# Kernel tuning notes

Hardware: AMD Instinct MI355X
Metric: run time of the kernel (lower is better)

Reference implementation:

```python
import jax, jax.numpy as jnp
import numpy as np

D = 512
N_CONCEPTS = 64
N_BANK = 200000
BS = 2048
N_CLASSES = 100
TOPK = 64


def setup_inputs() -> dict:
    key = jax.random.key(0)
    k1, k2, k3, k4 = jax.random.split(key, 4)
    concept = jax.random.uniform(k1, (D, N_CONCEPTS), dtype=jnp.float32, minval=-0.5, maxval=0.5)
    train_embedding = jax.random.normal(k2, (BS, D), dtype=jnp.float32)
    train_bank = jax.random.normal(k3, (N_BANK, D), dtype=jnp.float32)
    w_head = jax.random.normal(k4, (D, N_CLASSES), dtype=jnp.float32) * 0.05
    return {"concept": concept, "train_embedding": train_embedding,
            "train_bank": train_bank, "w_head": w_head, "topk": TOPK}


def reference(concept, train_embedding, train_bank, w_head, topk):
    # concept: (d, n_concepts); train_embedding: (bs, d); train_bank: (N, d)
    C = concept
    n_concepts = C.shape[1]
    gram = C.T @ C                                   # (n, n)
    proj_matrix = C @ jnp.linalg.inv(gram) @ C.T     # (d, d)
    modified = (proj_matrix @ train_embedding.T).T   # (bs, d) projected features
    # original_model modeled as linear head on the (hooked) bottleneck features
    y_pred = modified @ w_head                       # (bs, n_classes)
    orig_pred = train_embedding @ w_head             # (bs, n_classes)

    # vectorized per-concept euclidean distance to the whole bank + topk smallest
    bank_sq = jnp.sum(train_bank * train_bank, axis=1)        # (N,)
    c_sq = jnp.sum(C * C, axis=0)                             # (n,)
    d2 = c_sq[:, None] + bank_sq[None, :] - 2.0 * (C.T @ train_bank.T)  # (n, N)
    dist = jnp.sqrt(jnp.maximum(d2, 0.0))
    _, knn_idx = jax.lax.top_k(-dist, topk)                   # (n, k) smallest distances
    knn = train_bank[knn_idx]                                 # (n, k, d)
    dots = jnp.einsum('nkd,dn->n', knn, C) / topk             # sum(c * c_knn) / k per concept
    L_sparse_1 = jnp.mean(dots)

    eye = jnp.eye(n_concepts, dtype=gram.dtype)
    L_sparse_2 = jnp.mean(gram * (1.0 - eye))
    norm_metrics = jnp.mean(gram * eye)

    concept_pred = train_embedding @ C               # (bs, n_concepts)
    return (orig_pred, y_pred, L_sparse_1, L_sparse_2, norm_metrics, concept_pred)
```

## Files before the change

### kernel.cpp

```cpp
#include <hip/hip_runtime.h>
#include <float.h>

#define D_DIM 512
#define NC    64
#define NB    200000
#define BS_N  2048
#define NCL   100
#define TK    64
#define CAP   2048

#define O_ORIG 0
#define O_YPRED 204800
#define O_L1   409600
#define O_L2   409601
#define O_NORM 409602
#define O_CPRED 409603

#define W_GRAM  0
#define W_GINV  4096
#define W_U     8192
#define W_H     14592
#define W_Q     20992
#define W_MIN   220992
#define W_MAX   221056
#define W_BIN   221120
#define W_NBEL  221184
#define W_CCNT  221248
#define W_PSUM  221312
#define W_HIST  221376
#define W_CANDV 286912
#define W_CANDD 417984
#define W_PACKA 549056
#define W_PACKB 565440
#define W_S     610496

typedef __attribute__((ext_vector_type(8))) short bf16x8;
typedef __attribute__((ext_vector_type(4))) float f32x4;

__device__ inline unsigned f2ord(float f) {
    unsigned u = __float_as_uint(f);
    return (u & 0x80000000u) ? ~u : (u | 0x80000000u);
}
__device__ inline float ord2f(unsigned u) {
    return (u & 0x80000000u) ? __uint_as_float(u & 0x7fffffffu) : __uint_as_float(~u);
}
__device__ inline short f2bf(float f) {
    unsigned u = __float_as_uint(f);
    u += 0x7FFFu + ((u >> 16) & 1u);
    return (short)(u >> 16);
}

__global__ __launch_bounds__(256) void k1_setup(
    const float* __restrict__ C, const float* __restrict__ W,
    short* __restrict__ PA, short* __restrict__ PB,
    float* __restrict__ gram, float* __restrict__ U,
    unsigned* __restrict__ mnord, unsigned* __restrict__ mxord,
    unsigned* __restrict__ hist, int* __restrict__ ccnt, float* __restrict__ psum)
{
    int bid = blockIdx.x, t = threadIdx.x;
    if (bid < 16) {
        int idx = bid * 256 + t;
        int i = idx >> 6, j = idx & 63;
        float s = 0.f;
        for (int k = 0; k < D_DIM; ++k) s = fmaf(C[k*NC + i], C[k*NC + j], s);
        gram[idx] = s;
    } else if (bid < 41) {
        int idx = (bid - 16) * 256 + t;
        int i = idx / 100, j = idx - i * 100;
        float s = 0.f;
        for (int k = 0; k < D_DIM; ++k) s = fmaf(C[k*NC + i], W[k*NCL + j], s);
        U[idx] = s;
    } else if (bid < 281) {
        int b = bid - 41;
        #pragma unroll
        for (int rep = 0; rep < 2; ++rep) {
            int idx = t * 2 + rep;
            int lane = idx >> 3, j = idx & 7;
            if (b < 64) {
                int kt = b >> 2, ci = b & 3;
                int k = kt * 32 + (lane >> 4) * 8 + j;
                int col = ci * 16 + (lane & 15);
                PA[b * 512 + idx] = f2bf(C[k * NC + col]);
            } else {
                int bb = b - 64;
                int kt = bb / 11, ci = bb % 11;
                int k = kt * 32 + (lane >> 4) * 8 + j;
                int col = ci * 16 + (lane & 15);
                float v = 0.f;
                if (col < 64) v = C[k * NC + col];
                else if (col < 164) v = W[k * NCL + (col - 64)];
                PB[bb * 512 + idx] = f2bf(v);
            }
        }
    } else if (bid < 345) {
        int base = (bid - 281) * 1024;
        #pragma unroll
        for (int r = 0; r < 4; ++r) hist[base + r * 256 + t] = 0u;
    } else {
        if (t < 64) {
            mnord[t] = 0xFFFFFFFFu;
            mxord[t] = 0u;
            ccnt[t]  = 0;
            psum[t]  = 0.f;
        }
    }
}

__global__ __launch_bounds__(256) void k2_main(
    const float* __restrict__ E, const float* __restrict__ Bk,
    const short* __restrict__ PA, const short* __restrict__ PB,
    const float* __restrict__ gram, float* __restrict__ ginv,
    float* __restrict__ out3, float* __restrict__ T, float* __restrict__ O,
    float* __restrict__ S, float* __restrict__ Q,
    unsigned* __restrict__ mnord, unsigned* __restrict__ mxord)
{
    __shared__ float smem[64 * 65 + 64];
    int bid = blockIdx.x, t = threadIdx.x;

    if (bid == 0) {
        float (*A)[65] = (float(*)[65])smem;
        float* m = smem + 64 * 65;
        for (int idx = t; idx < 4096; idx += 256) A[idx >> 6][idx & 63] = gram[idx];
        __syncthreads();
        for (int k = 0; k < 64; ++k) {
            float d = 1.0f / A[k][k];
            if (t < 64) m[t] = A[t][k];
            __syncthreads();
            if (t < 64 && t != k) A[k][t] *= d;
            __syncthreads();
            for (int idx = t; idx < 4096; idx += 256) {
                int i = idx >> 6, j = idx & 63;
                if (i != k && j != k) A[i][j] = fmaf(-m[i], A[k][j], A[i][j]);
            }
            if (t < 64) {
                if (t != k) A[t][k] = -m[t] * d;
                else        A[k][k] = d;
            }
            __syncthreads();
        }
        for (int idx = t; idx < 4096; idx += 256) ginv[idx] = A[idx >> 6][idx & 63];
    } else if (bid == 1) {
        float* ra = smem; float* rd = smem + 256;
        float sa = 0.f, sd = 0.f;
        for (int idx = t; idx < NC * NC; idx += 256) {
            float g = gram[idx];
            sa += g;
            if (idx % (NC + 1) == 0) sd += g;
        }
        ra[t] = sa; rd[t] = sd;
        __syncthreads();
        for (int s2 = 128; s2 > 0; s2 >>= 1) {
            if (t < s2) { ra[t] += ra[t + s2]; rd[t] += rd[t + s2]; }
            __syncthreads();
        }
        if (t == 0) {
            out3[0] = 0.f;
            out3[1] = (ra[0] - rd[0]) * (1.0f / 4096.0f);
            out3[2] = rd[0] * (1.0f / 4096.0f);
        }
    } else if (bid < 18) {
        int eb = bid - 2;
        int wave = t >> 6, lane = t & 63;
        int quad = lane >> 4, l16 = lane & 15;
        int rbase = eb * 128 + wave * 32;
        int row0 = rbase + l16, row1 = rbase + 16 + l16;
        const float* p0 = E + (size_t)row0 * D_DIM + quad * 8;
        const float* p1 = E + (size_t)row1 * D_DIM + quad * 8;

        f32x4 acc[11][2];
        #pragma unroll
        for (int ci = 0; ci < 11; ++ci) { acc[ci][0] = 0.f; acc[ci][1] = 0.f; }

        for (int kt = 0; kt < 16; ++kt) {
            float4 a0 = *(const float4*)(p0 + kt*32);
            float4 b0 = *(const float4*)(p0 + kt*32 + 4);
            float4 a1 = *(const float4*)(p1 + kt*32);
            float4 b1 = *(const float4*)(p1 + kt*32 + 4);
            bf16x8 bf0 = { f2bf(a0.x), f2bf(a0.y), f2bf(a0.z), f2bf(a0.w),
                           f2bf(b0.x), f2bf(b0.y), f2bf(b0.z), f2bf(b0.w) };
            bf16x8 bf1 = { f2bf(a1.x), f2bf(a1.y), f2bf(a1.z), f2bf(a1.w),
                           f2bf(b1.x), f2bf(b1.y), f2bf(b1.z), f2bf(b1.w) };
            #pragma unroll
            for (int ci = 0; ci < 11; ++ci) {
                bf16x8 af = *(const bf16x8*)(PB + ((kt*11 + ci)*64 + lane)*8);
                acc[ci][0] = __builtin_amdgcn_mfma_f32_16x16x32_bf16(af, bf0, acc[ci][0], 0, 0, 0);
                acc[ci][1] = __builtin_amdgcn_mfma_f32_16x16x32_bf16(af, bf1, acc[ci][1], 0, 0, 0);
            }
        }
        #pragma unroll
        for (int ci = 0; ci < 11; ++ci) {
            #pragma unroll
            for (int j = 0; j < 4; ++j) {
                int col = ci*16 + quad*4 + j;
                if (col < 64) {
                    T[row0*NC + col] = acc[ci][0][j];
                    T[row1*NC + col] = acc[ci][1][j];
                } else if (col < 164) {
                    O[row0*NCL + (col-64)] = acc[ci][0][j];
                    O[row1*NCL + (col-64)] = acc[ci][1][j];
                }
            }
        }
    } else {
        int sb = bid - 18;
        unsigned* lmn = (unsigned*)smem;
        unsigned* lmx = lmn + 64;
        int wave = t >> 6, lane = t & 63;
        int quad = lane >> 4, l16 = lane & 15;
        if (t < 64) { lmn[t] = 0xFFFFFFFFu; lmx[t] = 0u; }
        __syncthreads();

        int rbase = sb * 128 + wave * 32;
        int row0 = rbase + l16, row1 = rbase + 16 + l16;
        bool v0 = row0 < NB, v1 = row1 < NB;
        int r0c = v0 ? row0 : (NB-1), r1c = v1 ? row1 : (NB-1);
        const float* p0 = Bk + (size_t)r0c * D_DIM + quad * 8;
        const float* p1 = Bk + (size_t)r1c * D_DIM + quad * 8;

        f32x4 acc[4][2];
        #pragma unroll
        for (int ci = 0; ci < 4; ++ci) { acc[ci][0] = 0.f; acc[ci][1] = 0.f; }
        float q0 = 0.f, q1 = 0.f;

        for (int kt = 0; kt < 16; ++kt) {
            float4 a0 = *(const float4*)(p0 + kt*32);
            float4 b0 = *(const float4*)(p0 + kt*32 + 4);
            float4 a1 = *(const float4*)(p1 + kt*32);
            float4 b1 = *(const float4*)(p1 + kt*32 + 4);
            q0 = fmaf(a0.x,a0.x, fmaf(a0.y,a0.y, fmaf(a0.z,a0.z, fmaf(a0.w,a0.w, q0))));
            q0 = fmaf(b0.x,b0.x, fmaf(b0.y,b0.y, fmaf(b0.z,b0.z, fmaf(b0.w,b0.w, q0))));
            q1 = fmaf(a1.x,a1.x, fmaf(a1.y,a1.y, fmaf(a1.z,a1.z, fmaf(a1.w,a1.w, q1))));
            q1 = fmaf(b1.x,b1.x, fmaf(b1.y,b1.y, fmaf(b1.z,b1.z, fmaf(b1.w,b1.w, q1))));
            bf16x8 bf0 = { f2bf(a0.x), f2bf(a0.y), f2bf(a0.z), f2bf(a0.w),
                           f2bf(b0.x), f2bf(b0.y), f2bf(b0.z), f2bf(b0.w) };
            bf16x8 bf1 = { f2bf(a1.x), f2bf(a1.y), f2bf(a1.z), f2bf(a1.w),
                           f2bf(b1.x), f2bf(b1.y), f2bf(b1.z), f2bf(b1.w) };
            #pragma unroll
            for (int ci = 0; ci < 4; ++ci) {
                bf16x8 af = *(const bf16x8*)(PA + ((kt*4 + ci)*64 + lane)*8);
                acc[ci][0] = __builtin_amdgcn_mfma_f32_16x16x32_bf16(af, bf0, acc[ci][0], 0, 0, 0);
                acc[ci][1] = __builtin_amdgcn_mfma_f32_16x16x32_bf16(af, bf1, acc[ci][1], 0, 0, 0);
            }
        }
        q0 += __shfl_xor(q0, 16); q0 += __shfl_xor(q0, 32);
        q1 += __shfl_xor(q1, 16); q1 += __shfl_xor(q1, 32);
        if (quad == 0) {
            if (v0) Q[row0] = q0;
            if (v1) Q[row1] = q1;
        }
        #pragma unroll
        for (int ci = 0; ci < 4; ++ci) {
            #pragma unroll
            for (int j = 0; j < 4; ++j) {
                int c = ci*16 + quad*4 + j;
                float s0 = q0 - 2.0f * acc[ci][0][j];
                float s1 = q1 - 2.0f * acc[ci][1][j];
                if (v0) S[(size_t)c*NB + row0] = s0;
                if (v1) S[(size_t)c*NB + row1] = s1;
                float mnv = fminf(v0 ? s0 : FLT_MAX,  v1 ? s1 : FLT_MAX);
                float mxv = fmaxf(v0 ? s0 : -FLT_MAX, v1 ? s1 : -FLT_MAX);
                #pragma unroll
                for (int o = 1; o < 16; o <<= 1) {
                    mnv = fminf(mnv, __shfl_xor(mnv, o));
                    mxv = fmaxf(mxv, __shfl_xor(mxv, o));
                }
                if (l16 == 0) {
                    atomicMin(&lmn[c], f2ord(mnv));
                    atomicMax(&lmx[c], f2ord(mxv));
                }
            }
        }
        __syncthreads();
        if (t < 64) {
            atomicMin(&mnord[t], lmn[t]);
            atomicMax(&mxord[t], lmx[t]);
        }
    }
}

__global__ __launch_bounds__(256) void k3_ph(
    const float* __restrict__ T, const float* __restrict__ ginv,
    const float* __restrict__ U, float* __restrict__ Y,
    const float* __restrict__ S, const unsigned* __restrict__ mnord,
    const unsigned* __restrict__ mxord, unsigned* __restrict__ hist)
{
    __shared__ float smem[6400];
    int bid = blockIdx.x, t = threadIdx.x;
    if (bid < 64) {
        for (int idx = t; idx < 6400; idx += 256) {
            int k = idx / 100, c = idx - k * 100;
            float s = 0.f;
            #pragma unroll 8
            for (int l = 0; l < NC; ++l) s = fmaf(ginv[k*NC + l], U[l*NCL + c], s);
            smem[idx] = s;
        }
        __syncthreads();
        for (int o = t; o < 3200; o += 256) {
            int r = o / 100, c = o - r * 100;
            int row = bid * 32 + r;
            float s = 0.f;
            #pragma unroll 8
            for (int k = 0; k < NC; ++k) s = fmaf(T[row*NC + k], smem[k*100 + c], s);
            Y[row*NCL + c] = s;
        }
    } else {
        int h = bid - 64;
        int c = h & 63, chunk = h >> 6;
        unsigned* hh = (unsigned*)smem;
        for (int i = t; i < 1024; i += 256) hh[i] = 0u;
        float mnf = ord2f(mnord[c]);
        float mxf = ord2f(mxord[c]);
        float invw = (mxf > mnf) ? 1024.0f / (mxf - mnf) : 0.f;
        __syncthreads();
        const float4* s4 = (const float4*)(S + (size_t)c * NB);
        int base = chunk * 1024;
        #pragma unroll
        for (int j = 0; j < 4; ++j) {
            int idx = base + j*256 + t;
            if (idx < NB/4) {
                float4 v = s4[idx];
                float vv[4] = {v.x, v.y, v.z, v.w};
                #pragma unroll
                for (int e = 0; e < 4; ++e) {
                    int b = (int)((vv[e] - mnf) * invw);
                    b = b < 0 ? 0 : (b > 1023 ? 1023 : b);
                    atomicAdd(&hh[b], 1u);
                }
            }
        }
        __syncthreads();
        for (int i = t; i < 1024; i += 256)
            if (hh[i]) atomicAdd(&hist[c*1024 + i], hh[i]);
    }
}

__global__ void scan_kernel(const unsigned* __restrict__ hist,
                            int* __restrict__ binB, int* __restrict__ nbel) {
    __shared__ unsigned h[1024];
    int c = blockIdx.x, t = threadIdx.x;
    for (int i = t; i < 1024; i += 256) h[i] = hist[c*1024 + i];
    __syncthreads();
    if (t == 0) {
        unsigned cum = 0; int B = 1023; unsigned below = 0;
        for (int b = 0; b < 1024; ++b) {
            unsigned hb = h[b];
            if (cum + hb >= TK) { B = b; below = cum; break; }
            cum += hb;
        }
        binB[c] = B;
        nbel[c] = (int)below;
    }
}

__global__ void collect_kernel(const float* __restrict__ S, const float* __restrict__ Q,
                               const unsigned* __restrict__ mn_ord, const unsigned* __restrict__ mx_ord,
                               const int* __restrict__ binB,
                               int* __restrict__ ccnt, float* __restrict__ candv,
                               float* __restrict__ candd, float* __restrict__ psum) {
    __shared__ float red[256];
    int c = blockIdx.y, t = threadIdx.x;
    float mnf = ord2f(mn_ord[c]);
    float mxf = ord2f(mx_ord[c]);
    float invw = (mxf > mnf) ? 1024.0f / (mxf - mnf) : 0.f;
    int B = binB[c];
    const float4* s4 = (const float4*)(S + (size_t)c * NB);
    int base = blockIdx.x * 1024;
    float dsum = 0.f;
    #pragma unroll
    for (int j = 0; j < 4; ++j) {
        int idx = base + j*256 + t;
        if (idx < NB/4) {
            float4 v = s4[idx];
            float vv[4] = {v.x, v.y, v.z, v.w};
            #pragma unroll
            for (int e = 0; e < 4; ++e) {
                int b = (int)((vv[e] - mnf) * invw);
                b = b < 0 ? 0 : (b > 1023 ? 1023 : b);
                if (b < B) {
                    dsum += (Q[idx*4 + e] - vv[e]) * 0.5f;
                } else if (b == B) {
                    int p = atomicAdd(&ccnt[c], 1);
                    if (p < CAP) {
                        candv[c*CAP + p] = vv[e];
                        candd[c*CAP + p] = (Q[idx*4 + e] - vv[e]) * 0.5f;
                    }
                }
            }
        }
    }
    red[t] = dsum;
    __syncthreads();
    for (int s2 = 128; s2 > 0; s2 >>= 1) {
        if (t < s2) red[t] += red[t+s2];
        __syncthreads();
    }
    if (t == 0 && red[0] != 0.f) atomicAdd(&psum[c], red[0]);
}

__global__ void final_kernel(const int* __restrict__ binB, const int* __restrict__ nbel,
                             const int* __restrict__ ccnt, const float* __restrict__ candv,
                             const float* __restrict__ candd, const float* __restrict__ psum,
                             float* __restrict__ out_l1) {
    __shared__ float v[CAP];
    __shared__ float dd[CAP];
    int c = blockIdx.x, t = threadIdx.x;
    int M = ccnt[c]; if (M > CAP) M = CAP;
    int r = TK - nbel[c]; if (r > M) r = M;
    for (int i = t; i < M; i += 64) { v[i] = candv[c*CAP + i]; dd[i] = candd[c*CAP + i]; }
    __syncthreads();
    float sum = 0.f;
    for (int j = 0; j < r; ++j) {
        float bv = FLT_MAX; int bi = -1;
        for (int i = t; i < M; i += 64)
            if (v[i] < bv) { bv = v[i]; bi = i; }
        #pragma unroll
        for (int o = 32; o > 0; o >>= 1) {
            float ov = __shfl_down(bv, o);
            int   oi = __shfl_down(bi, o);
            if (ov < bv) { bv = ov; bi = oi; }
        }
        bi = __shfl(bi, 0);
        if (t == 0 && bi >= 0) { sum += dd[bi]; v[bi] = FLT_MAX; }
        __syncthreads();
    }
    if (t == 0) atomicAdd(out_l1, (sum + psum[c]) * (1.0f/4096.0f));
}

extern "C" void kernel_launch(void* const* d_in, const int* in_sizes, int n_in,
                              void* d_out, int out_size, void* d_ws, size_t ws_size,
                              hipStream_t stream) {
    const float* C  = (const float*)d_in[0];
    const float* E  = (const float*)d_in[1];
    const float* Bk = (const float*)d_in[2];
    const float* W  = (const float*)d_in[3];
    float* out = (float*)d_out;
    float* ws  = (float*)d_ws;

    float*    gram  = ws + W_GRAM;
    float*    ginv  = ws + W_GINV;
    float*    U     = ws + W_U;
    float*    Q     = ws + W_Q;
    unsigned* mnord = (unsigned*)(ws + W_MIN);
    unsigned* mxord = (unsigned*)(ws + W_MAX);
    int*      binB  = (int*)(ws + W_BIN);
    int*      nbel  = (int*)(ws + W_NBEL);
    int*      ccnt  = (int*)(ws + W_CCNT);
    float*    psum  = ws + W_PSUM;
    unsigned* hist  = (unsigned*)(ws + W_HIST);
    float*    candv = ws + W_CANDV;
    float*    candd = ws + W_CANDD;
    short*    PA    = (short*)(ws + W_PACKA);
    short*    PB    = (short*)(ws + W_PACKB);
    float*    S     = ws + W_S;

    k1_setup<<<346, 256, 0, stream>>>(C, W, PA, PB, gram, U, mnord, mxord, hist, ccnt, psum);
    k2_main <<<1581, 256, 0, stream>>>(E, Bk, PA, PB, gram, ginv, out + O_L1,
                                       out + O_CPRED, out + O_ORIG, S, Q, mnord, mxord);
    k3_ph   <<<3200, 256, 0, stream>>>(out + O_CPRED, ginv, U, out + O_YPRED,
                                       S, mnord, mxord, hist);
    scan_kernel   <<<64, 256, 0, stream>>>(hist, binB, nbel);
    collect_kernel<<<dim3(49, 64), 256, 0, stream>>>(S, Q, mnord, mxord, binB, ccnt, candv, candd, psum);
    final_kernel  <<<NC, 64, 0, stream>>>(binB, nbel, ccnt, candv, candd, psum, out + O_L1);
}
```

Measured before the change: 703.1 us.

## Fold histogram scan into collect/final kernels and precompute ginv·U once

Removes the separate single-threaded scan kernel. collect_kernel and final_kernel now each run a parallel prefix scan over the histogram to find the threshold bin, so the sequential 1024-step loop and one launch go away. The ginv·U product is now computed once by the block that inverts the gram matrix, instead of redundantly in each of the 64 Y blocks of k3. final_kernel also moves to 256 threads, with a cross-wave argmin done through shared memory. The cost is a redundant scan in each of the 3136 collect blocks, plus extra serial work on the inversion block in k2.

```diff
diff --git a/kernel.cpp b/kernel.cpp
--- a/kernel.cpp
+++ b/kernel.cpp
@@ -23,7 +23,7 @@
 #define W_Q     20992
 #define W_MIN   220992
 #define W_MAX   221056
-#define W_BIN   221120
+#define W_DONE  221120
 #define W_NBEL  221184
 #define W_CCNT  221248
 #define W_PSUM  221312
@@ -109,7 +109,8 @@
 __global__ __launch_bounds__(256) void k2_main(
     const float* __restrict__ E, const float* __restrict__ Bk,
     const short* __restrict__ PA, const short* __restrict__ PB,
-    const float* __restrict__ gram, float* __restrict__ ginv,
+    const float* __restrict__ gram, const float* __restrict__ U,
+    float* __restrict__ ginv, float* __restrict__ H,
     float* __restrict__ out3, float* __restrict__ T, float* __restrict__ O,
     float* __restrict__ S, float* __restrict__ Q,
     unsigned* __restrict__ mnord, unsigned* __restrict__ mxord)
@@ -139,6 +140,13 @@
             __syncthreads();
         }
         for (int idx = t; idx < 4096; idx += 256) ginv[idx] = A[idx >> 6][idx & 63];
+        for (int idx = t; idx < 6400; idx += 256) {
+            int k = idx / 100, c = idx - k * 100;
+            float s = 0.f;
+            #pragma unroll 8
+            for (int l = 0; l < NC; ++l) s = fmaf(A[k][l], U[l*NCL + c], s);
+            H[idx] = s;
+        }
     } else if (bid == 1) {
         float* ra = smem; float* rd = smem + 256;
         float sa = 0.f, sd = 0.f;
@@ -279,21 +287,15 @@
 }
 
 __global__ __launch_bounds__(256) void k3_ph(
-    const float* __restrict__ T, const float* __restrict__ ginv,
-    const float* __restrict__ U, float* __restrict__ Y,
+    const float* __restrict__ T, const float* __restrict__ H,
+    float* __restrict__ Y,
     const float* __restrict__ S, const unsigned* __restrict__ mnord,
     const unsigned* __restrict__ mxord, unsigned* __restrict__ hist)
 {
     __shared__ float smem[6400];
     int bid = blockIdx.x, t = threadIdx.x;
     if (bid < 64) {
-        for (int idx = t; idx < 6400; idx += 256) {
-            int k = idx / 100, c = idx - k * 100;
-            float s = 0.f;
-            #pragma unroll 8
-            for (int l = 0; l < NC; ++l) s = fmaf(ginv[k*NC + l], U[l*NCL + c], s);
-            smem[idx] = s;
-        }
+        for (int idx = t; idx < 6400; idx += 256) smem[idx] = H[idx];
         __syncthreads();
         for (int o = t; o < 3200; o += 256) {
             int r = o / 100, c = o - r * 100;
@@ -334,35 +336,44 @@
     }
 }
 
-__global__ void scan_kernel(const unsigned* __restrict__ hist,
-                            int* __restrict__ binB, int* __restrict__ nbel) {
-    __shared__ unsigned h[1024];
-    int c = blockIdx.x, t = threadIdx.x;
-    for (int i = t; i < 1024; i += 256) h[i] = hist[c*1024 + i];
-    __syncthreads();
-    if (t == 0) {
-        unsigned cum = 0; int B = 1023; unsigned below = 0;
-        for (int b = 0; b < 1024; ++b) {
-            unsigned hb = h[b];
-            if (cum + hb >= TK) { B = b; below = cum; break; }
-            cum += hb;
-        }
-        binB[c] = B;
-        nbel[c] = (int)below;
-    }
-}
-
-__global__ void collect_kernel(const float* __restrict__ S, const float* __restrict__ Q,
-                               const unsigned* __restrict__ mn_ord, const unsigned* __restrict__ mx_ord,
-                               const int* __restrict__ binB,
-                               int* __restrict__ ccnt, float* __restrict__ candv,
-                               float* __restrict__ candd, float* __restrict__ psum) {
-    __shared__ float red[256];
+__global__ __launch_bounds__(256) void collect_kernel(
+    const float* __restrict__ S, const float* __restrict__ Q,
+    const unsigned* __restrict__ mn_ord, const unsigned* __restrict__ mx_ord,
+    const unsigned* __restrict__ hist,
+    int* __restrict__ ccnt, float* __restrict__ candv, float* __restrict__ candd,
+    float* __restrict__ psum)
+{
+    __shared__ float smem[256];
+    __shared__ int sB;
     int c = blockIdx.y, t = threadIdx.x;
+
+    {
+        unsigned* sc = (unsigned*)smem;
+        unsigned b4[4];
+        #pragma unroll
+        for (int i = 0; i < 4; ++i) b4[i] = hist[c*1024 + t*4 + i];
+        unsigned ts = b4[0] + b4[1] + b4[2] + b4[3];
+        sc[t] = ts;
+        __syncthreads();
+        for (int off = 1; off < 256; off <<= 1) {
+            unsigned v = (t >= off) ? sc[t - off] : 0u;
+            __syncthreads();
+            sc[t] += v;
+            __syncthreads();
+        }
+        unsigned cum = sc[t] - ts;
+        #pragma unroll
+        for (int i = 0; i < 4; ++i) {
+            if (cum < TK && cum + b4[i] >= TK) sB = t*4 + i;
+            cum += b4[i];
+        }
+        __syncthreads();
+    }
+    int B = sB;
+
     float mnf = ord2f(mn_ord[c]);
     float mxf = ord2f(mx_ord[c]);
     float invw = (mxf > mnf) ? 1024.0f / (mxf - mnf) : 0.f;
-    int B = binB[c];
     const float4* s4 = (const float4*)(S + (size_t)c * NB);
     int base = blockIdx.x * 1024;
     float dsum = 0.f;
@@ -388,30 +399,62 @@
             }
         }
     }
-    red[t] = dsum;
+
+    __syncthreads();
+    smem[t] = dsum;
     __syncthreads();
     for (int s2 = 128; s2 > 0; s2 >>= 1) {
-        if (t < s2) red[t] += red[t+s2];
-        __syncthreads();
-    }
-    if (t == 0 && red[0] != 0.f) atomicAdd(&psum[c], red[0]);
-}
-
-__global__ void final_kernel(const int* __restrict__ binB, const int* __restrict__ nbel,
-                             const int* __restrict__ ccnt, const float* __restrict__ candv,
-                             const float* __restrict__ candd, const float* __restrict__ psum,
-                             float* __restrict__ out_l1) {
+        if (t < s2) smem[t] += smem[t + s2];
+        __syncthreads();
+    }
+    if (t == 0 && smem[0] != 0.f) atomicAdd(&psum[c], smem[0]);
+}
+
+__global__ __launch_bounds__(256) void final_kernel(
+    const unsigned* __restrict__ hist,
+    const int* __restrict__ ccnt, const float* __restrict__ candv,
+    const float* __restrict__ candd, const float* __restrict__ psum,
+    float* __restrict__ out_l1)
+{
     __shared__ float v[CAP];
     __shared__ float dd[CAP];
+    __shared__ int sB, sNbel;
+    __shared__ float rv[4]; __shared__ int ri[4];
     int c = blockIdx.x, t = threadIdx.x;
+    int wave = t >> 6, lane = t & 63;
+
+    {
+        unsigned* sc = (unsigned*)v;
+        unsigned b4[4];
+        #pragma unroll
+        for (int i = 0; i < 4; ++i) b4[i] = hist[c*1024 + t*4 + i];
+        unsigned ts = b4[0] + b4[1] + b4[2] + b4[3];
+        sc[t] = ts;
+        __syncthreads();
+        for (int off = 1; off < 256; off <<= 1) {
+            unsigned x = (t >= off) ? sc[t - off] : 0u;
+            __syncthreads();
+            sc[t] += x;
+            __syncthreads();
+        }
+        unsigned cum = sc[t] - ts;
+        #pragma unroll
+        for (int i = 0; i < 4; ++i) {
+            if (cum < TK && cum + b4[i] >= TK) { sB = t*4 + i; sNbel = (int)cum; }
+            cum += b4[i];
+        }
+        __syncthreads();
+    }
+    int nbel = sNbel;
+
     int M = ccnt[c]; if (M > CAP) M = CAP;
-    int r = TK - nbel[c]; if (r > M) r = M;
-    for (int i = t; i < M; i += 64) { v[i] = candv[c*CAP + i]; dd[i] = candd[c*CAP + i]; }
+    int r = TK - nbel; if (r > M) r = M;
+    for (int i = t; i < M; i += 256) { v[i] = candv[c*CAP + i]; dd[i] = candd[c*CAP + i]; }
     __syncthreads();
     float sum = 0.f;
     for (int j = 0; j < r; ++j) {
         float bv = FLT_MAX; int bi = -1;
-        for (int i = t; i < M; i += 64)
+        for (int i = t; i < M; i += 256)
             if (v[i] < bv) { bv = v[i]; bi = i; }
         #pragma unroll
         for (int o = 32; o > 0; o >>= 1) {
@@ -419,8 +462,15 @@
             int   oi = __shfl_down(bi, o);
             if (ov < bv) { bv = ov; bi = oi; }
         }
-        bi = __shfl(bi, 0);
-        if (t == 0 && bi >= 0) { sum += dd[bi]; v[bi] = FLT_MAX; }
+        if (lane == 0) { rv[wave] = bv; ri[wave] = bi; }
+        __syncthreads();
+        if (t == 0) {
+            float bbv = rv[0]; int bbi = ri[0];
+            #pragma unroll
+            for (int w = 1; w < 4; ++w)
+                if (rv[w] < bbv) { bbv = rv[w]; bbi = ri[w]; }
+            if (bbi >= 0) { sum += dd[bbi]; v[bbi] = FLT_MAX; }
+        }
         __syncthreads();
     }
     if (t == 0) atomicAdd(out_l1, (sum + psum[c]) * (1.0f/4096.0f));
@@ -439,11 +489,10 @@
     float*    gram  = ws + W_GRAM;
     float*    ginv  = ws + W_GINV;
     float*    U     = ws + W_U;
+    float*    H     = ws + W_H;
     float*    Q     = ws + W_Q;
     unsigned* mnord = (unsigned*)(ws + W_MIN);
     unsigned* mxord = (unsigned*)(ws + W_MAX);
-    int*      binB  = (int*)(ws + W_BIN);
-    int*      nbel  = (int*)(ws + W_NBEL);
     int*      ccnt  = (int*)(ws + W_CCNT);
     float*    psum  = ws + W_PSUM;
     unsigned* hist  = (unsigned*)(ws + W_HIST);
@@ -454,11 +503,11 @@
     float*    S     = ws + W_S;
 
     k1_setup<<<346, 256, 0, stream>>>(C, W, PA, PB, gram, U, mnord, mxord, hist, ccnt, psum);
-    k2_main <<<1581, 256, 0, stream>>>(E, Bk, PA, PB, gram, ginv, out + O_L1,
+    k2_main <<<1581, 256, 0, stream>>>(E, Bk, PA, PB, gram, U, ginv, H, out + O_L1,
                                        out + O_CPRED, out + O_ORIG, S, Q, mnord, mxord);
-    k3_ph   <<<3200, 256, 0, stream>>>(out + O_CPRED, ginv, U, out + O_YPRED,
+    k3_ph   <<<3200, 256, 0, stream>>>(out + O_CPRED, H, out + O_YPRED,
                                        S, mnord, mxord, hist);
-    scan_kernel   <<<64, 256, 0, stream>>>(hist, binB, nbel);
-    collect_kernel<<<dim3(49, 64), 256, 0, stream>>>(S, Q, mnord, mxord, binB, ccnt, candv, candd, psum);
-    final_kernel  <<<NC, 64, 0, stream>>>(binB, nbel, ccnt, candv, candd, psum, out + O_L1);
-}
+    collect_kernel<<<dim3(49, 64), 256, 0, stream>>>(S, Q, mnord, mxord, hist,
+                                                     ccnt, candv, candd, psum);
+    final_kernel  <<<NC, 256, 0, stream>>>(hist, ccnt, candv, candd, psum, out + O_L1);
+}
```

Result: faster. 660.3 us (-6.1%).
